# Optimization experiments

Measured on AMD Instinct MI355X. Metric: run time of the kernel, lower is better.

The kernel has to match this reference:

```python
import jax, jax.numpy as jnp
import numpy as np

TINY = float(np.finfo(np.float32).tiny)


def setup_inputs() -> dict:
    key = jax.random.key(0)
    ks = jax.random.split(key, 8)
    B, T, Qd, Vd, D = 32, 8192, 512, 256, 128
    query = jax.random.normal(ks[0], (B, Qd), jnp.float32)
    value = jax.random.normal(ks[1], (B, T, Vd), jnp.float32)
    previous_alignment = jax.random.uniform(ks[2], (B, T), jnp.float32)
    # normalize to a valid alignment distribution per row (as in real decoding)
    previous_alignment = previous_alignment / jnp.sum(previous_alignment, axis=-1, keepdims=True)
    Wq = jax.random.normal(ks[3], (Qd, D), jnp.float32) * 0.02
    bq = jnp.zeros((D,), jnp.float32)
    Wv = jax.random.normal(ks[4], (Vd, D), jnp.float32) * 0.02
    bv = jnp.zeros((D,), jnp.float32)
    attention_v = jax.random.normal(ks[5], (D,), jnp.float32) * 0.1
    score_bias = jnp.zeros((), jnp.float32)
    return dict(query=query, value=value, previous_alignment=previous_alignment,
                Wq=Wq, bq=bq, Wv=Wv, bv=bv, attention_v=attention_v,
                score_bias=score_bias)


def reference(query, value, previous_alignment, Wq, bq, Wv, bv, attention_v, score_bias):
    # Query/Value dense projections (3-input form: key == projected value)
    q = query @ Wq + bq                                   # [B, D]
    v = value @ Wv + bv                                   # [B, T, D]
    # Bahdanau additive score: sum(v_att * tanh(q + k), -1) + bias -> [B, T]
    score = jnp.einsum('d,btd->bt', attention_v, jnp.tanh(q[:, None, :] + v)) + score_bias
    # Monotonic attention (recursive form, parallelized via cumsum/cumprod)
    p = jax.nn.sigmoid(score)                             # p_choose_i
    logs = jnp.log(jnp.clip(1.0 - p, TINY, 1.0))
    # exclusive safe cumprod of (1 - p): exp(exclusive cumsum of log)
    cp = jnp.exp(jnp.cumsum(logs, axis=-1) - logs)        # [B, T]
    alignment = p * cp * jnp.cumsum(
        previous_alignment / jnp.clip(cp, 1e-10, 1.0), axis=-1)
    # context = alignment @ projected value -> [B, D]
    context = jnp.einsum('bt,btd->bd', alignment, v)
    return context, alignment
```

## Files before the change

### kernel.cpp

```cpp
#include <hip/hip_runtime.h>
#include <hip/hip_bf16.h>
#include <math.h>

#define BB   32
#define TT_  8192
#define QD   512
#define VD   256
#define DD   128
#define TINYF 1.17549435e-38f

#define TTILE 64
#define CCH   32

#define TSPEC_CHUNKS 2
#define TSPEC (TSPEC_CHUNKS*256)
#define TSPEC_TILES (TSPEC/TTILE)

__global__ __launch_bounds__(128) void k_qproj(
    const float* __restrict__ query, const float* __restrict__ Wq,
    const float* __restrict__ bq, float* __restrict__ qout) {
  int b = blockIdx.x, d = threadIdx.x;
  __shared__ float qrow[QD];
  for (int c = threadIdx.x; c < QD; c += 128) qrow[c] = query[b*QD + c];
  __syncthreads();
  float acc = bq[d];
  #pragma unroll 8
  for (int c = 0; c < QD; ++c) acc = fmaf(qrow[c], Wq[c*DD + d], acc);
  qout[b*DD + d] = acc;
}

__global__ __launch_bounds__(256) void k_score(
    const float* __restrict__ value, const float* __restrict__ Wv,
    const float* __restrict__ bv, const float* __restrict__ qv,
    const float* __restrict__ attv, const float* __restrict__ sbias,
    float* __restrict__ score, int t_tile_base, const int* __restrict__ flags) {
  int b = blockIdx.y;
  if (flags && flags[b] == 0) return;
  int t0 = (t_tile_base + blockIdx.x) * TTILE;
  int tid = threadIdx.x;
  int dq = tid & 31;
  int tq = tid >> 5;

  __shared__ float WvL[CCH * DD];
  __shared__ float valT[CCH * 68];

  float acc[8][4];
  #pragma unroll
  for (int i = 0; i < 8; ++i)
    #pragma unroll
    for (int j = 0; j < 4; ++j) acc[i][j] = 0.f;

  const float* vbase = value + ((size_t)b * TT_ + t0) * VD;

  for (int c0 = 0; c0 < VD; c0 += CCH) {
    const float4* wsrc = (const float4*)(Wv + (size_t)c0 * DD);
    float4* wdst = (float4*)WvL;
    #pragma unroll
    for (int k = 0; k < 4; ++k) wdst[tid + 256 * k] = wsrc[tid + 256 * k];
    #pragma unroll
    for (int k = 0; k < 2; ++k) {
      int id = tid * 2 + k;
      int tt = id >> 3;
      int c4 = id & 7;
      float4 vv = *(const float4*)(vbase + (size_t)tt * VD + c0 + c4 * 4);
      int cr = c4 * 4;
      valT[(cr + 0) * 68 + tt] = vv.x;
      valT[(cr + 1) * 68 + tt] = vv.y;
      valT[(cr + 2) * 68 + tt] = vv.z;
      valT[(cr + 3) * 68 + tt] = vv.w;
    }
    __syncthreads();
    #pragma unroll 4
    for (int cc = 0; cc < CCH; ++cc) {
      const float4 wv  = *(const float4*)(&WvL[cc * DD + dq * 4]);
      const float4 va0 = *(const float4*)(&valT[cc * 68 + tq * 8]);
      const float4 va1 = *(const float4*)(&valT[cc * 68 + tq * 8 + 4]);
      float va[8] = {va0.x, va0.y, va0.z, va0.w, va1.x, va1.y, va1.z, va1.w};
      #pragma unroll
      for (int i = 0; i < 8; ++i) {
        acc[i][0] = fmaf(va[i], wv.x, acc[i][0]);
        acc[i][1] = fmaf(va[i], wv.y, acc[i][1]);
        acc[i][2] = fmaf(va[i], wv.z, acc[i][2]);
        acc[i][3] = fmaf(va[i], wv.w, acc[i][3]);
      }
    }
    __syncthreads();
  }

  float sb = sbias[0];
  float qd[4], av[4], bvv[4];
  #pragma unroll
  for (int j = 0; j < 4; ++j) {
    int d = dq * 4 + j;
    qd[j]  = qv[b * DD + d];
    av[j]  = attv[d];
    bvv[j] = bv[d];
  }
  #pragma unroll
  for (int i = 0; i < 8; ++i) {
    float s = 0.f;
    #pragma unroll
    for (int j = 0; j < 4; ++j) {
      float x = qd[j] + acc[i][j] + bvv[j];
      s += av[j] * tanhf(x);
    }
    #pragma unroll
    for (int m = 16; m >= 1; m >>= 1) s += __shfl_xor(s, m, 64);
    if (dq == 0) score[(size_t)b * TT_ + t0 + tq * 8 + i] = s + sb;
  }
}

__global__ __launch_bounds__(256) void k_scan(
    const float* __restrict__ score, const float* __restrict__ prev,
    float* __restrict__ align_out, float* __restrict__ suma,
    float* __restrict__ carryLs, float* __restrict__ carryDs,
    int* __restrict__ flags, int chunk0, int nchunks, int phase) {
  int b = blockIdx.x, tid = threadIdx.x;
  int lane = tid & 63, w = tid >> 6;
  __shared__ float wsA[4], wsB[4];

  float cL, cD, sacc;
  if (phase == 1) {
    if (flags[b] == 0) return;
    cL = carryLs[b]; cD = carryDs[b]; sacc = suma[b];
  } else {
    cL = 0.f; cD = 0.f; sacc = 0.f;
  }

  const size_t base = (size_t)b * TT_;
  for (int ch = 0; ch < nchunks; ++ch) {
    int t = (chunk0 + ch) * 256 + tid;
    float s = score[base + t];
    float p  = 1.f / (1.f + expf(-s));
    float om = 1.f / (1.f + expf(s));
    float l = logf(fmaxf(om, TINYF));

    float inc = l;
    #pragma unroll
    for (int o = 1; o < 64; o <<= 1) {
      float n = __shfl_up(inc, o, 64);
      if (lane >= o) inc += n;
    }
    if (lane == 63) wsA[w] = inc;
    __syncthreads();
    float off = 0.f;
    #pragma unroll
    for (int j = 0; j < 4; ++j) if (j < w) off += wsA[j];
    float totA = wsA[0] + wsA[1] + wsA[2] + wsA[3];
    float cums = cL + off + inc;
    float cp = expf(cums - l);
    float den = prev[base + t] / fminf(fmaxf(cp, 1e-10f), 1.f);

    float inc2 = den;
    #pragma unroll
    for (int o = 1; o < 64; o <<= 1) {
      float n = __shfl_up(inc2, o, 64);
      if (lane >= o) inc2 += n;
    }
    if (lane == 63) wsB[w] = inc2;
    __syncthreads();
    float off2 = 0.f;
    #pragma unroll
    for (int j = 0; j < 4; ++j) if (j < w) off2 += wsB[j];
    float totB = wsB[0] + wsB[1] + wsB[2] + wsB[3];

    float a = p * cp * (cD + off2 + inc2);
    align_out[base + t] = a;
    sacc += a;
    cL += totA; cD += totB;
    __syncthreads();
  }

  #pragma unroll
  for (int o = 32; o >= 1; o >>= 1) sacc += __shfl_xor(sacc, o, 64);
  if (lane == 0) wsA[w] = sacc;
  __syncthreads();
  float stot = wsA[0] + wsA[1] + wsA[2] + wsA[3];

  if (phase == 0) {
    bool done = (expf(cL) == 0.f);
    if (done) {
      int tstart = (chunk0 + nchunks) * 256;
      float4 z = make_float4(0.f, 0.f, 0.f, 0.f);
      float4* dst = (float4*)(align_out + base + tstart);
      int n4 = (TT_ - tstart) / 4;
      for (int i = tid; i < n4; i += 256) dst[i] = z;
      if (tid == 0) { flags[b] = 0; suma[b] = stot; }
    } else {
      if (tid == 0) { flags[b] = 1; suma[b] = stot; carryLs[b] = cL; carryDs[b] = cD; }
    }
  } else {
    if (tid == 0) suma[b] = stot;
  }
}

__global__ __launch_bounds__(256) void k_u(
    const float* __restrict__ value, const float* __restrict__ align,
    float* __restrict__ u) {
  int b = blockIdx.y, chunk = blockIdx.x, c = threadIdx.x;
  __shared__ float aL[256];
  __shared__ int any;
  if (c == 0) any = 0;
  __syncthreads();
  int t0 = chunk * 256;
  float av = align[(size_t)b * TT_ + t0 + c];
  aL[c] = av;
  if (av != 0.f) any = 1;
  __syncthreads();
  if (!any) return;
  const float* vp = value + ((size_t)b * TT_ + t0) * VD + c;
  float acc = 0.f;
  #pragma unroll 8
  for (int i = 0; i < 256; ++i) acc = fmaf(aL[i], vp[(size_t)i * VD], acc);
  atomicAdd(&u[b * VD + c], acc);
}

__global__ __launch_bounds__(128) void k_ctx(
    const float* __restrict__ u, const float* __restrict__ Wv,
    const float* __restrict__ bv, const float* __restrict__ suma,
    float* __restrict__ ctx) {
  int b = blockIdx.x, d = threadIdx.x;
  __shared__ float uL[VD];
  uL[d] = u[b * VD + d];
  uL[d + 128] = u[b * VD + d + 128];
  __syncthreads();
  float acc = suma[b] * bv[d];
  #pragma unroll 8
  for (int c = 0; c < VD; ++c) acc = fmaf(uL[c], Wv[c * DD + d], acc);
  ctx[b * DD + d] = acc;
}

extern "C" void kernel_launch(void* const* d_in, const int* in_sizes, int n_in,
                              void* d_out, int out_size, void* d_ws, size_t ws_size,
                              hipStream_t stream) {
  const float* query = (const float*)d_in[0];
  const float* value = (const float*)d_in[1];
  const float* prev  = (const float*)d_in[2];
  const float* Wq    = (const float*)d_in[3];
  const float* bq    = (const float*)d_in[4];
  const float* Wv    = (const float*)d_in[5];
  const float* bv    = (const float*)d_in[6];
  const float* attv  = (const float*)d_in[7];
  const float* sbias = (const float*)d_in[8];

  float* ctx_out   = (float*)d_out;
  float* align_out = (float*)d_out + BB * DD;

  float* ws = (float*)d_ws;
  float* q      = ws;
  float* score  = ws + 4096;
  float* suma   = ws + 266240;
  float* carryL = ws + 266272;
  float* carryD = ws + 266304;
  int*   flags  = (int*)(ws + 266336);
  float* u      = ws + 266368;

  hipMemsetAsync(u, 0, BB * VD * sizeof(float), stream);

  k_qproj<<<BB, 128, 0, stream>>>(query, Wq, bq, q);

  k_score<<<dim3(TSPEC_TILES, BB), 256, 0, stream>>>(
      value, Wv, bv, q, attv, sbias, score, 0, nullptr);

  k_scan<<<BB, 256, 0, stream>>>(score, prev, align_out, suma,
                                 carryL, carryD, flags, 0, TSPEC_CHUNKS, 0);

  k_score<<<dim3(TT_ / TTILE - TSPEC_TILES, BB), 256, 0, stream>>>(
      value, Wv, bv, q, attv, sbias, score, TSPEC_TILES, flags);

  k_scan<<<BB, 256, 0, stream>>>(score, prev, align_out, suma,
                                 carryL, carryD, flags, TSPEC_CHUNKS,
                                 TT_ / 256 - TSPEC_CHUNKS, 1);

  k_u<<<dim3(TT_ / 256, BB), 256, 0, stream>>>(value, align_out, u);

  k_ctx<<<BB, 128, 0, stream>>>(u, Wv, bv, suma, ctx_out);
}
```

Measured before the change: 404.8 us.

## Fuse query projection into score, fuse scan with context for early-saturated rows

Removes the separate query-projection kernel by recomputing q inside each score block. The speculative prefix shrinks from 512 to 256 timesteps. The first scan kernel now also computes the alignment-weighted value sum and the context projection whenever the cumulative product has already underflowed, so the later kernels exit early. The memset, atomic u kernel and separate ctx kernel are replaced by a per-row fallback kernel. The cost is redundant Wq work in every score block and a serial fallback path if rows don't saturate.

New measurement: 476.1 us. 17.6% more time.

```diff
diff --git a/kernel.cpp b/kernel.cpp
--- a/kernel.cpp
+++ b/kernel.cpp
@@ -12,32 +12,39 @@
 #define TTILE 64
 #define CCH   32
 
-#define TSPEC_CHUNKS 2
-#define TSPEC (TSPEC_CHUNKS*256)
-#define TSPEC_TILES (TSPEC/TTILE)
-
-__global__ __launch_bounds__(128) void k_qproj(
-    const float* __restrict__ query, const float* __restrict__ Wq,
-    const float* __restrict__ bq, float* __restrict__ qout) {
-  int b = blockIdx.x, d = threadIdx.x;
-  __shared__ float qrow[QD];
-  for (int c = threadIdx.x; c < QD; c += 128) qrow[c] = query[b*QD + c];
-  __syncthreads();
-  float acc = bq[d];
-  #pragma unroll 8
-  for (int c = 0; c < QD; ++c) acc = fmaf(qrow[c], Wq[c*DD + d], acc);
-  qout[b*DD + d] = acc;
-}
+#define TSPEC 256
+#define TSPEC_TILES (TSPEC / TTILE)
 
 __global__ __launch_bounds__(256) void k_score(
-    const float* __restrict__ value, const float* __restrict__ Wv,
-    const float* __restrict__ bv, const float* __restrict__ qv,
+    const float* __restrict__ value, const float* __restrict__ query,
+    const float* __restrict__ Wq, const float* __restrict__ bq,
+    const float* __restrict__ Wv, const float* __restrict__ bv,
     const float* __restrict__ attv, const float* __restrict__ sbias,
     float* __restrict__ score, int t_tile_base, const int* __restrict__ flags) {
   int b = blockIdx.y;
   if (flags && flags[b] == 0) return;
+  int tid = threadIdx.x;
+
+  __shared__ float qrow[QD];
+  __shared__ float qpart[2][DD];
+  __shared__ float qsh[DD];
+  qrow[tid]       = query[b * QD + tid];
+  qrow[tid + 256] = query[b * QD + tid + 256];
+  __syncthreads();
+  {
+    int h = tid >> 7, d = tid & 127;
+    const float* wq = Wq + (size_t)(h * 256) * DD + d;
+    const float* qr = qrow + h * 256;
+    float acc = 0.f;
+    #pragma unroll 8
+    for (int c = 0; c < 256; ++c) acc = fmaf(qr[c], wq[(size_t)c * DD], acc);
+    qpart[h][d] = acc;
+  }
+  __syncthreads();
+  if (tid < DD) qsh[tid] = qpart[0][tid] + qpart[1][tid] + bq[tid] + bv[tid];
+  __syncthreads();
+
   int t0 = (t_tile_base + blockIdx.x) * TTILE;
-  int tid = threadIdx.x;
   int dq = tid & 31;
   int tq = tid >> 5;
 
@@ -88,20 +95,19 @@
   }
 
   float sb = sbias[0];
-  float qd[4], av[4], bvv[4];
+  float qd[4], av[4];
   #pragma unroll
   for (int j = 0; j < 4; ++j) {
     int d = dq * 4 + j;
-    qd[j]  = qv[b * DD + d];
-    av[j]  = attv[d];
-    bvv[j] = bv[d];
+    qd[j] = qsh[d];
+    av[j] = attv[d];
   }
   #pragma unroll
   for (int i = 0; i < 8; ++i) {
     float s = 0.f;
     #pragma unroll
     for (int j = 0; j < 4; ++j) {
-      float x = qd[j] + acc[i][j] + bvv[j];
+      float x = qd[j] + acc[i][j];
       s += av[j] * tanhf(x);
     }
     #pragma unroll
@@ -110,24 +116,104 @@
   }
 }
 
-__global__ __launch_bounds__(256) void k_scan(
+__global__ __launch_bounds__(256) void k_scan0_uctx(
+    const float* __restrict__ score, const float* __restrict__ prev,
+    const float* __restrict__ value, const float* __restrict__ Wv,
+    const float* __restrict__ bv,
+    float* __restrict__ align_out, float* __restrict__ ctx,
+    float* __restrict__ suma, float* __restrict__ carryL,
+    float* __restrict__ carryD, int* __restrict__ flags) {
+  int b = blockIdx.x, tid = threadIdx.x;
+  int lane = tid & 63, w = tid >> 6;
+  __shared__ float wsA[4], wsB[4], wsS[4];
+  __shared__ float aL[256];
+  __shared__ float uL[256];
+  const size_t base = (size_t)b * TT_;
+
+  float s = score[base + tid];
+  float p  = 1.f / (1.f + expf(-s));
+  float om = 1.f / (1.f + expf(s));
+  float l = logf(fmaxf(om, TINYF));
+
+  float inc = l;
+  #pragma unroll
+  for (int o = 1; o < 64; o <<= 1) {
+    float n = __shfl_up(inc, o, 64);
+    if (lane >= o) inc += n;
+  }
+  if (lane == 63) wsA[w] = inc;
+  __syncthreads();
+  float off = 0.f;
+  #pragma unroll
+  for (int j = 0; j < 4; ++j) if (j < w) off += wsA[j];
+  float totA = wsA[0] + wsA[1] + wsA[2] + wsA[3];
+  float cums = off + inc;
+  float cp = expf(cums - l);
+  float den = prev[base + tid] / fminf(fmaxf(cp, 1e-10f), 1.f);
+
+  float inc2 = den;
+  #pragma unroll
+  for (int o = 1; o < 64; o <<= 1) {
+    float n = __shfl_up(inc2, o, 64);
+    if (lane >= o) inc2 += n;
+  }
+  if (lane == 63) wsB[w] = inc2;
+  __syncthreads();
+  float off2 = 0.f;
+  #pragma unroll
+  for (int j = 0; j < 4; ++j) if (j < w) off2 += wsB[j];
+  float totB = wsB[0] + wsB[1] + wsB[2] + wsB[3];
+
+  float a = p * cp * (off2 + inc2);
+  align_out[base + tid] = a;
+  aL[tid] = a;
+
+  float sa = a;
+  #pragma unroll
+  for (int o = 32; o >= 1; o >>= 1) sa += __shfl_xor(sa, o, 64);
+  if (lane == 0) wsS[w] = sa;
+  __syncthreads();
+  float stot = wsS[0] + wsS[1] + wsS[2] + wsS[3];
+
+  bool done = (expf(totA) == 0.f);
+  if (!done) {
+    if (tid == 0) { flags[b] = 1; suma[b] = stot; carryL[b] = totA; carryD[b] = totB; }
+    return;
+  }
+  if (tid == 0) { flags[b] = 0; suma[b] = stot; }
+
+  float4 z = make_float4(0.f, 0.f, 0.f, 0.f);
+  float4* dst = (float4*)(align_out + base + TSPEC);
+  for (int i = tid; i < (TT_ - TSPEC) / 4; i += 256) dst[i] = z;
+
+  const float* vp = value + base * VD + tid;
+  float acc = 0.f;
+  #pragma unroll 8
+  for (int t = 0; t < TSPEC; ++t) acc = fmaf(aL[t], vp[(size_t)t * VD], acc);
+  uL[tid] = acc;
+  __syncthreads();
+
+  if (tid < DD) {
+    float c = stot * bv[tid];
+    #pragma unroll 8
+    for (int cc = 0; cc < VD; ++cc) c = fmaf(uL[cc], Wv[cc * DD + tid], c);
+    ctx[b * DD + tid] = c;
+  }
+}
+
+__global__ __launch_bounds__(256) void k_scan1(
     const float* __restrict__ score, const float* __restrict__ prev,
     float* __restrict__ align_out, float* __restrict__ suma,
-    float* __restrict__ carryLs, float* __restrict__ carryDs,
-    int* __restrict__ flags, int chunk0, int nchunks, int phase) {
+    const float* __restrict__ carryL, const float* __restrict__ carryD,
+    const int* __restrict__ flags) {
   int b = blockIdx.x, tid = threadIdx.x;
+  if (flags[b] == 0) return;
   int lane = tid & 63, w = tid >> 6;
   __shared__ float wsA[4], wsB[4];
-
-  float cL, cD, sacc;
-  if (phase == 1) {
-    if (flags[b] == 0) return;
-    cL = carryLs[b]; cD = carryDs[b]; sacc = suma[b];
-  } else {
-    cL = 0.f; cD = 0.f; sacc = 0.f;
-  }
-
+  float cL = carryL[b], cD = carryD[b], sacc = suma[b];
   const size_t base = (size_t)b * TT_;
+  const int chunk0 = TSPEC / 256, nchunks = TT_ / 256 - TSPEC / 256;
+
   for (int ch = 0; ch < nchunks; ++ch) {
     int t = (chunk0 + ch) * 256 + tid;
     float s = score[base + t];
@@ -175,59 +261,43 @@
   for (int o = 32; o >= 1; o >>= 1) sacc += __shfl_xor(sacc, o, 64);
   if (lane == 0) wsA[w] = sacc;
   __syncthreads();
-  float stot = wsA[0] + wsA[1] + wsA[2] + wsA[3];
-
-  if (phase == 0) {
-    bool done = (expf(cL) == 0.f);
-    if (done) {
-      int tstart = (chunk0 + nchunks) * 256;
-      float4 z = make_float4(0.f, 0.f, 0.f, 0.f);
-      float4* dst = (float4*)(align_out + base + tstart);
-      int n4 = (TT_ - tstart) / 4;
-      for (int i = tid; i < n4; i += 256) dst[i] = z;
-      if (tid == 0) { flags[b] = 0; suma[b] = stot; }
-    } else {
-      if (tid == 0) { flags[b] = 1; suma[b] = stot; carryLs[b] = cL; carryDs[b] = cD; }
-    }
-  } else {
-    if (tid == 0) suma[b] = stot;
-  }
-}
-
-__global__ __launch_bounds__(256) void k_u(
+  if (tid == 0) suma[b] = wsA[0] + wsA[1] + wsA[2] + wsA[3];
+}
+
+__global__ __launch_bounds__(256) void k_uctx_fb(
     const float* __restrict__ value, const float* __restrict__ align,
-    float* __restrict__ u) {
-  int b = blockIdx.y, chunk = blockIdx.x, c = threadIdx.x;
+    const float* __restrict__ Wv, const float* __restrict__ bv,
+    const float* __restrict__ suma, float* __restrict__ ctx,
+    const int* __restrict__ flags) {
+  int b = blockIdx.x, tid = threadIdx.x;
+  if (flags[b] == 0) return;
   __shared__ float aL[256];
+  __shared__ float uL[256];
   __shared__ int any;
-  if (c == 0) any = 0;
-  __syncthreads();
-  int t0 = chunk * 256;
-  float av = align[(size_t)b * TT_ + t0 + c];
-  aL[c] = av;
-  if (av != 0.f) any = 1;
-  __syncthreads();
-  if (!any) return;
-  const float* vp = value + ((size_t)b * TT_ + t0) * VD + c;
+  const size_t base = (size_t)b * TT_;
   float acc = 0.f;
-  #pragma unroll 8
-  for (int i = 0; i < 256; ++i) acc = fmaf(aL[i], vp[(size_t)i * VD], acc);
-  atomicAdd(&u[b * VD + c], acc);
-}
-
-__global__ __launch_bounds__(128) void k_ctx(
-    const float* __restrict__ u, const float* __restrict__ Wv,
-    const float* __restrict__ bv, const float* __restrict__ suma,
-    float* __restrict__ ctx) {
-  int b = blockIdx.x, d = threadIdx.x;
-  __shared__ float uL[VD];
-  uL[d] = u[b * VD + d];
-  uL[d + 128] = u[b * VD + d + 128];
-  __syncthreads();
-  float acc = suma[b] * bv[d];
-  #pragma unroll 8
-  for (int c = 0; c < VD; ++c) acc = fmaf(uL[c], Wv[c * DD + d], acc);
-  ctx[b * DD + d] = acc;
+  for (int ch = 0; ch < TT_ / 256; ++ch) {
+    if (tid == 0) any = 0;
+    __syncthreads();
+    float a = align[base + ch * 256 + tid];
+    aL[tid] = a;
+    if (a != 0.f) any = 1;
+    __syncthreads();
+    if (any) {
+      const float* vp = value + (base + (size_t)ch * 256) * VD + tid;
+      #pragma unroll 8
+      for (int t = 0; t < 256; ++t) acc = fmaf(aL[t], vp[(size_t)t * VD], acc);
+    }
+    __syncthreads();
+  }
+  uL[tid] = acc;
+  __syncthreads();
+  if (tid < DD) {
+    float c = suma[b] * bv[tid];
+    #pragma unroll 8
+    for (int cc = 0; cc < VD; ++cc) c = fmaf(uL[cc], Wv[cc * DD + tid], c);
+    ctx[b * DD + tid] = c;
+  }
 }
 
 extern "C" void kernel_launch(void* const* d_in, const int* in_sizes, int n_in,
@@ -247,32 +317,25 @@
   float* align_out = (float*)d_out + BB * DD;
 
   float* ws = (float*)d_ws;
-  float* q      = ws;
-  float* score  = ws + 4096;
-  float* suma   = ws + 266240;
-  float* carryL = ws + 266272;
-  float* carryD = ws + 266304;
-  int*   flags  = (int*)(ws + 266336);
-  float* u      = ws + 266368;
-
-  hipMemsetAsync(u, 0, BB * VD * sizeof(float), stream);
-
-  k_qproj<<<BB, 128, 0, stream>>>(query, Wq, bq, q);
+  float* score  = ws;
+  float* suma   = ws + 262144;
+  float* carryL = ws + 262176;
+  float* carryD = ws + 262208;
+  int*   flags  = (int*)(ws + 262240);
 
   k_score<<<dim3(TSPEC_TILES, BB), 256, 0, stream>>>(
-      value, Wv, bv, q, attv, sbias, score, 0, nullptr);
-
-  k_scan<<<BB, 256, 0, stream>>>(score, prev, align_out, suma,
-                                 carryL, carryD, flags, 0, TSPEC_CHUNKS, 0);
+      value, query, Wq, bq, Wv, bv, attv, sbias, score, 0, nullptr);
+
+  k_scan0_uctx<<<BB, 256, 0, stream>>>(score, prev, value, Wv, bv,
+                                       align_out, ctx_out, suma,
+                                       carryL, carryD, flags);
 
   k_score<<<dim3(TT_ / TTILE - TSPEC_TILES, BB), 256, 0, stream>>>(
-      value, Wv, bv, q, attv, sbias, score, TSPEC_TILES, flags);
-
-  k_scan<<<BB, 256, 0, stream>>>(score, prev, align_out, suma,
-                                 carryL, carryD, flags, TSPEC_CHUNKS,
-                                 TT_ / 256 - TSPEC_CHUNKS, 1);
-
-  k_u<<<dim3(TT_ / 256, BB), 256, 0, stream>>>(value, align_out, u);
-
-  k_ctx<<<BB, 128, 0, stream>>>(u, Wv, bv, suma, ctx_out);
-}
+      value, query, Wq, bq, Wv, bv, attv, sbias, score, TSPEC_TILES, flags);
+
+  k_scan1<<<BB, 256, 0, stream>>>(score, prev, align_out, suma,
+                                  carryL, carryD, flags);
+
+  k_uctx_fb<<<BB, 256, 0, stream>>>(value, align_out, Wv, bv, suma,
+                                    ctx_out, flags);
+}
```
